# Performance work log

Hardware: AMD Instinct MI355X
Metric: run time of the kernel (lower is better)

Reference implementation:

```python
import jax, jax.numpy as jnp
import numpy as np


def setup_inputs() -> dict:
    key = jax.random.key(0)
    ks = jax.random.split(key, 7)
    N, D, K = 500000, 128, 32
    return {
        "x": jax.random.normal(ks[0], (N, D), dtype=jnp.float32),
        "h_e": jax.random.normal(ks[1], (N, D), dtype=jnp.float32),
        "bond_n": jax.random.uniform(ks[2], (K, N), dtype=jnp.float32),
        "W_i_w": jax.random.normal(ks[3], (D, 2 * D), dtype=jnp.float32) * 0.05,
        "W_i_b": jax.random.normal(ks[4], (D,), dtype=jnp.float32) * 0.05,
        "W_m_w": jax.random.normal(ks[5], (D, D), dtype=jnp.float32) * 0.05,
        "W_m_b": jax.random.normal(ks[6], (D,), dtype=jnp.float32) * 0.05,
    }


def reference(x, h_e, bond_n, W_i_w, W_i_b, W_m_w, W_m_b):
    # h_n = relu(W_i([x ; h_e]))  -> [N, D]
    h_n = jax.nn.relu(jnp.concatenate([x, h_e], axis=1) @ W_i_w.T + W_i_b)
    # m = sum_k sum_n bond_n[k,n] * h_n[n,:]  -> [D]
    # (equivalent to torch: (bond_n[...,None] * h_n).sum(1).sum(0),
    #  but expressed as a contraction to avoid the [K,N,D] intermediate)
    m = jnp.einsum('kn,nd->d', bond_n, h_n)
    # h = relu(h_n + W_m(m))  -> [N, D] via broadcast of the [D] message
    h = jax.nn.relu(h_n + (m @ W_m_w.T + W_m_b))
    return h
```

## Files before the change

kernel.cpp:

```cpp
#include <hip/hip_runtime.h>
#include <stdint.h>
#include <stddef.h>

#define N_ROWS 500000
#define DDIM   128
#define K2     256
#define KBOND  32
#define TILE   32
#define NTL    (N_ROWS / TILE)
#define NBLK   1536
#define MR_BLKS 24
#define P2_BLOCKS 2048

typedef float  f32x4  __attribute__((ext_vector_type(4)));
typedef __bf16 bf16x8 __attribute__((ext_vector_type(8)));
typedef __bf16 bf16x4 __attribute__((ext_vector_type(4)));

__device__ __bf16 g_wbf[DDIM * K2];
__device__ float  g_s[N_ROWS];
__device__ float  g_partials[NBLK * DDIM];
__device__ float  g_p2[MR_BLKS * DDIM];
__device__ float  g_msg[DDIM];
__device__ __bf16 g_hn[(size_t)N_ROWS * DDIM];

__global__ void k_prep(const float* __restrict__ w) {
  int t = blockIdx.x * blockDim.x + threadIdx.x;
  if (t < DDIM * K2) g_wbf[t] = (__bf16)w[t];
}

__global__ __launch_bounds__(256)
void k_s(const float* __restrict__ bond) {
  int n = blockIdx.x * 256 + threadIdx.x;
  if (n >= N_ROWS) return;
  float a = 0.f, b = 0.f;
  #pragma unroll
  for (int k = 0; k < KBOND; k += 2) {
    a += bond[(size_t)k * N_ROWS + n];
    b += bond[(size_t)(k + 1) * N_ROWS + n];
  }
  g_s[n] = a + b;
}

__global__ __launch_bounds__(512)
void k_pass1(const float* __restrict__ x, const float* __restrict__ he,
             const float* __restrict__ bias)
{
  __shared__ __align__(16) unsigned char a_lds[2][TILE * 512];

  const int tid  = threadIdx.x;
  const int w    = tid >> 6;
  const int lane = tid & 63;
  const int l15  = lane & 15;
  const int g    = lane >> 4;

  bf16x8 wfrag[8];
  #pragma unroll
  for (int ks = 0; ks < 8; ++ks)
    wfrag[ks] = *(const bf16x8*)(g_wbf + (size_t)(16 * w + l15) * K2 + 32 * ks + 8 * g);

  const int d0 = 16 * w + 4 * g;
  const f32x4 bv = *(const f32x4*)(bias + d0);

  const int sr = tid >> 4;
  const int sc = tid & 15;
  const unsigned swz   = (unsigned)((sr & 15) << 4);
  const unsigned wo_x  = (unsigned)(sr * 512) + ((16u * sc) ^ swz);
  const unsigned wo_he = (unsigned)(sr * 512) + 256u + ((16u * sc) ^ swz);
  const unsigned rsw   = (unsigned)(l15 << 4);

  f32x4 macc = (f32x4)(0.f);

  int t = blockIdx.x;

  {
    const float* xr = x  + (size_t)(t * TILE + sr) * DDIM + 8 * sc;
    const float* hr = he + (size_t)(t * TILE + sr) * DDIM + 8 * sc;
    f32x4 xa = *(const f32x4*)xr, xb = *(const f32x4*)(xr + 4);
    f32x4 ha = *(const f32x4*)hr, hb = *(const f32x4*)(hr + 4);
    bf16x8 bx, bh;
    #pragma unroll
    for (int i = 0; i < 4; ++i) {
      bx[i] = (__bf16)xa[i]; bx[4 + i] = (__bf16)xb[i];
      bh[i] = (__bf16)ha[i]; bh[4 + i] = (__bf16)hb[i];
    }
    *(bf16x8*)(&a_lds[0][wo_x])  = bx;
    *(bf16x8*)(&a_lds[0][wo_he]) = bh;
  }
  float s0 = g_s[t * TILE + l15];
  float s1 = g_s[t * TILE + 16 + l15];
  __syncthreads();

  int cur = 0;
  while (true) {
    const int  tn  = t + NBLK;
    const bool has = tn < NTL;
    const int  tl  = has ? tn : t;

    const float* xr = x  + (size_t)(tl * TILE + sr) * DDIM + 8 * sc;
    const float* hr = he + (size_t)(tl * TILE + sr) * DDIM + 8 * sc;
    f32x4 xa = *(const f32x4*)xr, xb = *(const f32x4*)(xr + 4);
    f32x4 ha = *(const f32x4*)hr, hb = *(const f32x4*)(hr + 4);
    float s0n = g_s[tl * TILE + l15];
    float s1n = g_s[tl * TILE + 16 + l15];
    __builtin_amdgcn_sched_barrier(0);

    f32x4 acc0 = (f32x4)(0.f), acc1 = (f32x4)(0.f);
    const unsigned char* base = &a_lds[cur][0];
    #pragma unroll
    for (int ks = 0; ks < 8; ++ks) {
      const unsigned o = (unsigned)(64 * ks + 16 * g);
      bf16x8 b0 = *(const bf16x8*)(base + l15 * 512        + (o ^ rsw));
      bf16x8 b1 = *(const bf16x8*)(base + (16 + l15) * 512 + (o ^ rsw));
      acc0 = __builtin_amdgcn_mfma_f32_16x16x32_bf16(wfrag[ks], b0, acc0, 0, 0, 0);
      acc1 = __builtin_amdgcn_mfma_f32_16x16x32_bf16(wfrag[ks], b1, acc1, 0, 0, 0);
    }

    {
      const int rb = t * TILE;
      f32x4 h0, h1;
      #pragma unroll
      for (int i = 0; i < 4; ++i) {
        float a = acc0[i] + bv[i]; h0[i] = a > 0.f ? a : 0.f;
        float b = acc1[i] + bv[i]; h1[i] = b > 0.f ? b : 0.f;
      }
      #pragma unroll
      for (int i = 0; i < 4; ++i) macc[i] += s0 * h0[i] + s1 * h1[i];
      bf16x4 hb0, hb1;
      #pragma unroll
      for (int i = 0; i < 4; ++i) { hb0[i] = (__bf16)h0[i]; hb1[i] = (__bf16)h1[i]; }
      *(bf16x4*)(g_hn + (size_t)(rb + l15) * DDIM + d0)      = hb0;
      *(bf16x4*)(g_hn + (size_t)(rb + 16 + l15) * DDIM + d0) = hb1;
    }
    __builtin_amdgcn_sched_barrier(0);

    {
      bf16x8 bx, bh;
      #pragma unroll
      for (int i = 0; i < 4; ++i) {
        bx[i] = (__bf16)xa[i]; bx[4 + i] = (__bf16)xb[i];
        bh[i] = (__bf16)ha[i]; bh[4 + i] = (__bf16)hb[i];
      }
      *(bf16x8*)(&a_lds[cur ^ 1][wo_x])  = bx;
      *(bf16x8*)(&a_lds[cur ^ 1][wo_he]) = bh;
    }
    __syncthreads();

    if (!has) break;
    t = tn; cur ^= 1; s0 = s0n; s1 = s1n;
  }

  #pragma unroll
  for (int off = 1; off <= 8; off <<= 1) {
    #pragma unroll
    for (int i = 0; i < 4; ++i) macc[i] += __shfl_xor(macc[i], off, 64);
  }
  if (l15 == 0)
    *(f32x4*)(&g_partials[(size_t)blockIdx.x * DDIM + d0]) = macc;
}

__global__ void k_mr() {
  const int d    = threadIdx.x & 127;
  const int half = threadIdx.x >> 7;
  const int r0   = blockIdx.x * 64;
  float acc = 0.f;
  for (int r = r0 + half; r < r0 + 64; r += 2)
    acc += g_partials[(size_t)r * DDIM + d];
  __shared__ float sp[DDIM];
  if (half == 0) sp[d] = acc;
  __syncthreads();
  if (half == 1) g_p2[blockIdx.x * DDIM + d] = sp[d] + acc;
}

__global__ void k_msg(const float* __restrict__ wm, const float* __restrict__ bm) {
  __shared__ float ms[DDIM];
  const int d = threadIdx.x;
  float s = 0.f;
  #pragma unroll
  for (int c = 0; c < MR_BLKS; ++c) s += g_p2[c * DDIM + d];
  ms[d] = s;
  __syncthreads();
  float acc = bm[d];
  #pragma unroll 8
  for (int j = 0; j < DDIM; ++j) acc += ms[j] * wm[(size_t)d * DDIM + j];
  g_msg[d] = acc;
}

__global__ __launch_bounds__(256)
void k_pass2(float* __restrict__ out)
{
  __shared__ float ms[DDIM];
  if (threadIdx.x < DDIM) ms[threadIdx.x] = g_msg[threadIdx.x];
  __syncthreads();
  const size_t total = (size_t)N_ROWS * DDIM / 8;
  for (size_t c = (size_t)blockIdx.x * blockDim.x + threadIdx.x; c < total;
       c += (size_t)gridDim.x * blockDim.x) {
    const size_t base = c * 8;
    const int col0 = (int)(base & (DDIM - 1));
    bf16x8 hv = *(const bf16x8*)(g_hn + base);
    f32x4 o0, o1;
    #pragma unroll
    for (int i = 0; i < 4; ++i) {
      float a = (float)hv[i]     + ms[col0 + i];
      float b = (float)hv[4 + i] + ms[col0 + 4 + i];
      o0[i] = a > 0.f ? a : 0.f;
      o1[i] = b > 0.f ? b : 0.f;
    }
    *(f32x4*)(out + base)     = o0;
    *(f32x4*)(out + base + 4) = o1;
  }
}

extern "C" void kernel_launch(void* const* d_in, const int* in_sizes, int n_in,
                              void* d_out, int out_size, void* d_ws, size_t ws_size,
                              hipStream_t stream) {
  const float* x    = (const float*)d_in[0];
  const float* he   = (const float*)d_in[1];
  const float* bond = (const float*)d_in[2];
  const float* wi   = (const float*)d_in[3];
  const float* bi   = (const float*)d_in[4];
  const float* wm   = (const float*)d_in[5];
  const float* bm   = (const float*)d_in[6];
  float* out = (float*)d_out;
  (void)d_ws; (void)ws_size;

  k_prep<<<(DDIM * K2 + 255) / 256, 256, 0, stream>>>(wi);
  k_s<<<(N_ROWS + 255) / 256, 256, 0, stream>>>(bond);
  k_pass1<<<NBLK, 512, 0, stream>>>(x, he, bi);
  k_mr<<<MR_BLKS, 256, 0, stream>>>();
  k_msg<<<1, 128, 0, stream>>>(wm, bm);
  k_pass2<<<P2_BLOCKS, 256, 0, stream>>>(out);
}
```

Before: 266.5 us.

## Shrink pass1 tiles to 16 rows with 4 waves each covering 32 output columns

```diff
diff --git a/kernel.cpp b/kernel.cpp
--- a/kernel.cpp
+++ b/kernel.cpp
@@ -6,10 +6,10 @@
 #define DDIM   128
 #define K2     256
 #define KBOND  32
-#define TILE   32
+#define TILE   16
 #define NTL    (N_ROWS / TILE)
-#define NBLK   1536
-#define MR_BLKS 24
+#define NBLK   768
+#define MR_BLKS 12
 #define P2_BLOCKS 2048
 
 typedef float  f32x4  __attribute__((ext_vector_type(4)));
@@ -41,7 +41,7 @@
   g_s[n] = a + b;
 }
 
-__global__ __launch_bounds__(512)
+__global__ __launch_bounds__(256, 3)
 void k_pass1(const float* __restrict__ x, const float* __restrict__ he,
              const float* __restrict__ bias)
 {
@@ -53,23 +53,25 @@
   const int l15  = lane & 15;
   const int g    = lane >> 4;
 
-  bf16x8 wfrag[8];
-  #pragma unroll
-  for (int ks = 0; ks < 8; ++ks)
-    wfrag[ks] = *(const bf16x8*)(g_wbf + (size_t)(16 * w + l15) * K2 + 32 * ks + 8 * g);
-
-  const int d0 = 16 * w + 4 * g;
-  const f32x4 bv = *(const f32x4*)(bias + d0);
+  bf16x8 wfrag[2][8];
+  #pragma unroll
+  for (int dg = 0; dg < 2; ++dg)
+    #pragma unroll
+    for (int ks = 0; ks < 8; ++ks)
+      wfrag[dg][ks] = *(const bf16x8*)(g_wbf +
+          (size_t)(32 * w + 16 * dg + l15) * K2 + 32 * ks + 8 * g);
+
+  f32x4 bv0 = *(const f32x4*)(bias + 32 * w + 4 * g);
+  f32x4 bv1 = *(const f32x4*)(bias + 32 * w + 16 + 4 * g);
 
   const int sr = tid >> 4;
   const int sc = tid & 15;
-  const unsigned swz   = (unsigned)((sr & 15) << 4);
+  const unsigned swz   = (unsigned)(sr << 4);
   const unsigned wo_x  = (unsigned)(sr * 512) + ((16u * sc) ^ swz);
-  const unsigned wo_he = (unsigned)(sr * 512) + 256u + ((16u * sc) ^ swz);
+  const unsigned wo_he = (unsigned)(sr * 512) + ((256u + 16u * sc) ^ swz);
   const unsigned rsw   = (unsigned)(l15 << 4);
 
-  f32x4 macc = (f32x4)(0.f);
-
+  f32x4 macc0 = (f32x4)(0.f), macc1 = (f32x4)(0.f);
   int t = blockIdx.x;
 
   {
@@ -87,8 +89,10 @@
     *(bf16x8*)(&a_lds[0][wo_he]) = bh;
   }
   float s0 = g_s[t * TILE + l15];
-  float s1 = g_s[t * TILE + 16 + l15];
-  __syncthreads();
+  __builtin_amdgcn_sched_barrier(0);
+  asm volatile("s_waitcnt lgkmcnt(0)");
+  __builtin_amdgcn_s_barrier();
+  __builtin_amdgcn_sched_barrier(0);
 
   int cur = 0;
   while (true) {
@@ -101,7 +105,6 @@
     f32x4 xa = *(const f32x4*)xr, xb = *(const f32x4*)(xr + 4);
     f32x4 ha = *(const f32x4*)hr, hb = *(const f32x4*)(hr + 4);
     float s0n = g_s[tl * TILE + l15];
-    float s1n = g_s[tl * TILE + 16 + l15];
     __builtin_amdgcn_sched_barrier(0);
 
     f32x4 acc0 = (f32x4)(0.f), acc1 = (f32x4)(0.f);
@@ -109,27 +112,26 @@
     #pragma unroll
     for (int ks = 0; ks < 8; ++ks) {
       const unsigned o = (unsigned)(64 * ks + 16 * g);
-      bf16x8 b0 = *(const bf16x8*)(base + l15 * 512        + (o ^ rsw));
-      bf16x8 b1 = *(const bf16x8*)(base + (16 + l15) * 512 + (o ^ rsw));
-      acc0 = __builtin_amdgcn_mfma_f32_16x16x32_bf16(wfrag[ks], b0, acc0, 0, 0, 0);
-      acc1 = __builtin_amdgcn_mfma_f32_16x16x32_bf16(wfrag[ks], b1, acc1, 0, 0, 0);
+      bf16x8 b = *(const bf16x8*)(base + l15 * 512 + (o ^ rsw));
+      acc0 = __builtin_amdgcn_mfma_f32_16x16x32_bf16(wfrag[0][ks], b, acc0, 0, 0, 0);
+      acc1 = __builtin_amdgcn_mfma_f32_16x16x32_bf16(wfrag[1][ks], b, acc1, 0, 0, 0);
     }
 
     {
-      const int rb = t * TILE;
+      const int n = t * TILE + l15;
       f32x4 h0, h1;
       #pragma unroll
       for (int i = 0; i < 4; ++i) {
-        float a = acc0[i] + bv[i]; h0[i] = a > 0.f ? a : 0.f;
-        float b = acc1[i] + bv[i]; h1[i] = b > 0.f ? b : 0.f;
+        float a = acc0[i] + bv0[i]; h0[i] = a > 0.f ? a : 0.f;
+        float b = acc1[i] + bv1[i]; h1[i] = b > 0.f ? b : 0.f;
       }
       #pragma unroll
-      for (int i = 0; i < 4; ++i) macc[i] += s0 * h0[i] + s1 * h1[i];
+      for (int i = 0; i < 4; ++i) { macc0[i] += s0 * h0[i]; macc1[i] += s0 * h1[i]; }
       bf16x4 hb0, hb1;
       #pragma unroll
       for (int i = 0; i < 4; ++i) { hb0[i] = (__bf16)h0[i]; hb1[i] = (__bf16)h1[i]; }
-      *(bf16x4*)(g_hn + (size_t)(rb + l15) * DDIM + d0)      = hb0;
-      *(bf16x4*)(g_hn + (size_t)(rb + 16 + l15) * DDIM + d0) = hb1;
+      *(bf16x4*)(g_hn + (size_t)n * DDIM + 32 * w + 4 * g)      = hb0;
+      *(bf16x4*)(g_hn + (size_t)n * DDIM + 32 * w + 16 + 4 * g) = hb1;
     }
     __builtin_amdgcn_sched_barrier(0);
 
@@ -143,19 +145,27 @@
       *(bf16x8*)(&a_lds[cur ^ 1][wo_x])  = bx;
       *(bf16x8*)(&a_lds[cur ^ 1][wo_he]) = bh;
     }
-    __syncthreads();
+    __builtin_amdgcn_sched_barrier(0);
+    asm volatile("s_waitcnt lgkmcnt(0)");
+    __builtin_amdgcn_s_barrier();
+    __builtin_amdgcn_sched_barrier(0);
 
     if (!has) break;
-    t = tn; cur ^= 1; s0 = s0n; s1 = s1n;
+    t = tn; cur ^= 1; s0 = s0n;
   }
 
   #pragma unroll
   for (int off = 1; off <= 8; off <<= 1) {
     #pragma unroll
-    for (int i = 0; i < 4; ++i) macc[i] += __shfl_xor(macc[i], off, 64);
-  }
-  if (l15 == 0)
-    *(f32x4*)(&g_partials[(size_t)blockIdx.x * DDIM + d0]) = macc;
+    for (int i = 0; i < 4; ++i) {
+      macc0[i] += __shfl_xor(macc0[i], off, 64);
+      macc1[i] += __shfl_xor(macc1[i], off, 64);
+    }
+  }
+  if (l15 == 0) {
+    *(f32x4*)(&g_partials[(size_t)blockIdx.x * DDIM + 32 * w + 4 * g])      = macc0;
+    *(f32x4*)(&g_partials[(size_t)blockIdx.x * DDIM + 32 * w + 16 + 4 * g]) = macc1;
+  }
 }
 
 __global__ void k_mr() {
@@ -225,7 +235,7 @@
 
   k_prep<<<(DDIM * K2 + 255) / 256, 256, 0, stream>>>(wi);
   k_s<<<(N_ROWS + 255) / 256, 256, 0, stream>>>(bond);
-  k_pass1<<<NBLK, 512, 0, stream>>>(x, he, bi);
+  k_pass1<<<NBLK, 256, 0, stream>>>(x, he, bi);
   k_mr<<<MR_BLKS, 256, 0, stream>>>();
   k_msg<<<1, 128, 0, stream>>>(wm, bm);
   k_pass2<<<P2_BLOCKS, 256, 0, stream>>>(out);
```

Result: no change. 264.3 us (-0.8%).
